# Performance work log

Hardware: AMD Instinct MI355X
Metric: run time of the kernel (lower is better)

Reference implementation:

```python
import jax, jax.numpy as jnp
import numpy as np

B, S, H, W = 16, 4096, 1024, 1024


def setup_inputs() -> dict:
    key = jax.random.key(0)
    k1, k2, k3 = jax.random.split(key, 3)
    hidden_states = jax.random.normal(k1, (B, S, H), dtype=jnp.float32)
    # (start, end) spans with start <= end, indices in [0, S)
    word_idxs = jnp.sort(jax.random.randint(k2, (B, W, 2), 0, S), axis=-1)
    # number of valid words per example, in [1, W]
    max_word_len = jax.random.randint(k3, (B,), 1, W + 1)
    return {"hidden_states": hidden_states, "word_idxs": word_idxs,
            "max_word_len": max_word_len}


def reference(hidden_states, word_idxs, max_word_len):
    # hidden_states: (B, S, H); word_idxs: (B, W, 2) int; max_word_len: (B,) int
    b, s, h = hidden_states.shape
    w = word_idxs.shape[1]
    start = word_idxs[..., 0]                      # (B, W)
    end = word_idxs[..., 1]                        # (B, W)
    pos = jnp.arange(s)                            # (S,)
    # word k is valid iff k < max_word_len[b]
    valid = (jnp.arange(w)[None, :] < max_word_len[:, None])   # (B, W) bool
    # dense mean-pooling matrix: 1/len inside [start, end], 0 elsewhere
    inside = (pos[None, None, :] >= start[..., None]) & \
             (pos[None, None, :] <= end[..., None])            # (B, W, S)
    length = (end - start + 1).astype(hidden_states.dtype)     # >= 1 by construction
    pool = inside.astype(hidden_states.dtype) / length[..., None]
    pool = pool * valid[..., None].astype(hidden_states.dtype)
    word_embedding = jnp.einsum('bws,bsh->bwh', pool, hidden_states)
    word_masks = valid.astype(jnp.int64)
    return word_embedding, word_masks
```

## Files before the change

kernel.cpp:

```cpp
#include <hip/hip_runtime.h>

static constexpr int B = 16, S = 4096, H = 1024, W = 1024;
static constexpr int NC = 64;
static constexpr int CS = S / NC;
static constexpr int LOG2_CS = 6;
static constexpr int BMW = S / 32;

__global__ void k_bitset(const int* __restrict__ widx, const int* __restrict__ mwl,
                         unsigned* __restrict__ bm) {
    int tid = blockIdx.x * 256 + threadIdx.x;
    if (tid >= B * W) return;
    int b = tid / W, w = tid % W;
    if (w >= mwl[b]) return;
    int start = widx[tid * 2 + 0];
    int end   = widx[tid * 2 + 1];
    atomicOr(&bm[b * BMW + (end >> 5)], 1u << (end & 31));
    if (start > 0) {
        int sm = start - 1;
        atomicOr(&bm[b * BMW + (sm >> 5)], 1u << (sm & 31));
    }
}

__global__ void __launch_bounds__(256)
k_chunk_prefix(const float* __restrict__ hs, const unsigned* __restrict__ bm,
               float* __restrict__ L, float* __restrict__ CTraw) {
    int c = blockIdx.x % NC;
    int b = blockIdx.x / NC;
    int col = threadIdx.x * 4;
    size_t rowbase = ((size_t)b * S + (size_t)c * CS) * H + col;
    unsigned bw0 = bm[b * BMW + c * 2 + 0];
    unsigned bw1 = bm[b * BMW + c * 2 + 1];
    float4 acc = make_float4(0.f, 0.f, 0.f, 0.f);
#pragma unroll 8
    for (int s = 0; s < CS; ++s) {
        float4 v = *(const float4*)(hs + rowbase + (size_t)s * H);
        acc.x += v.x; acc.y += v.y; acc.z += v.z; acc.w += v.w;
        unsigned bits = (s < 32) ? (bw0 >> s) : (bw1 >> (s - 32));
        if (bits & 1u)
            *(float4*)(L + rowbase + (size_t)s * H) = acc;
    }
    *(float4*)(CTraw + ((size_t)b * NC + c) * H + col) = acc;
}

__global__ void k_coarse(const float* __restrict__ CTraw, float* __restrict__ CTp) {
    int hc = blockIdx.x % (H / 256);
    int b  = blockIdx.x / (H / 256);
    int h  = hc * 256 + threadIdx.x;
    float acc = 0.f;
#pragma unroll 8
    for (int c = 0; c < NC; ++c) {
        size_t idx = ((size_t)b * NC + c) * H + h;
        CTp[idx] = acc;
        acc += CTraw[idx];
    }
}

__global__ void __launch_bounds__(256)
k_gather(const float* __restrict__ L, const float* __restrict__ CTp,
         const int* __restrict__ widx, const int* __restrict__ mwl,
         float* __restrict__ out, float* __restrict__ mask) {
    int t = threadIdx.x;
    int wid = t >> 6, lane = t & 63;
    int word = blockIdx.x * 4 + wid;
    int b = word / W, w = word % W;
    size_t orow = (size_t)word * H;

    bool valid = (w < mwl[b]);
    if (lane == 0) mask[word] = valid ? 1.0f : 0.0f;

    if (!valid) {
        float4 z = make_float4(0.f, 0.f, 0.f, 0.f);
#pragma unroll
        for (int k = 0; k < 4; ++k)
            *(float4*)(out + orow + k * 256 + lane * 4) = z;
        return;
    }

    int start = widx[word * 2 + 0];
    int end   = widx[word * 2 + 1];
    float inv = 1.0f / (float)(end - start + 1);
    int ce = end >> LOG2_CS;
    const float* Le = L   + ((size_t)b * S + end) * H;
    const float* Ce = CTp + ((size_t)b * NC + ce) * H;
    bool has_s = (start > 0);
    const float* Ls = Le; const float* Cs = Ce;
    if (has_s) {
        int sm = start - 1, cs = sm >> LOG2_CS;
        Ls = L   + ((size_t)b * S + sm) * H;
        Cs = CTp + ((size_t)b * NC + cs) * H;
    }

#pragma unroll
    for (int k = 0; k < 4; ++k) {
        int off = k * 256 + lane * 4;
        float4 e  = *(const float4*)(Le + off);
        float4 ct = *(const float4*)(Ce + off);
        float sx = e.x + ct.x, sy = e.y + ct.y, sz = e.z + ct.z, sw = e.w + ct.w;
        if (has_s) {
            float4 s4 = *(const float4*)(Ls + off);
            float4 c4 = *(const float4*)(Cs + off);
            sx -= s4.x + c4.x; sy -= s4.y + c4.y; sz -= s4.z + c4.z; sw -= s4.w + c4.w;
        }
        float4 o = make_float4(sx * inv, sy * inv, sz * inv, sw * inv);
        *(float4*)(out + orow + off) = o;
    }
}

__global__ void k_direct(const float* __restrict__ hs, const int* __restrict__ widx,
                         const int* __restrict__ mwl, float* __restrict__ out,
                         float* __restrict__ mask) {
    int w = blockIdx.x % W;
    int b = blockIdx.x / W;
    int t = threadIdx.x;
    bool valid = (w < mwl[b]);
    size_t orow = ((size_t)b * W + w) * H;
    if (t == 0) mask[(size_t)b * W + w] = valid ? 1.0f : 0.0f;

    float4 acc = make_float4(0.f, 0.f, 0.f, 0.f);
    if (valid) {
        int start = widx[((size_t)b * W + w) * 2 + 0];
        int end   = widx[((size_t)b * W + w) * 2 + 1];
        float inv = 1.0f / (float)(end - start + 1);
        for (int s = start; s <= end; ++s) {
            const float4 v = *(const float4*)(hs + ((size_t)b * S + s) * H + (size_t)t * 4);
            acc.x += v.x; acc.y += v.y; acc.z += v.z; acc.w += v.w;
        }
        acc.x *= inv; acc.y *= inv; acc.z *= inv; acc.w *= inv;
    }
    *(float4*)(out + orow + (size_t)t * 4) = acc;
}

extern "C" void kernel_launch(void* const* d_in, const int* in_sizes, int n_in,
                              void* d_out, int out_size, void* d_ws, size_t ws_size,
                              hipStream_t stream) {
    const float* hs  = (const float*)d_in[0];
    const int*  widx = (const int*)d_in[1];
    const int*  mwl  = (const int*)d_in[2];
    float* out  = (float*)d_out;
    float* mask = out + (size_t)B * W * H;

    const size_t Lbytes  = (size_t)B * S * H * sizeof(float);
    const size_t CTbytes = (size_t)B * NC * H * sizeof(float);
    const size_t BMbytes = (size_t)B * BMW * sizeof(unsigned);

    if (ws_size >= Lbytes + 2 * CTbytes + BMbytes) {
        float* L      = (float*)d_ws;
        float* CTraw  = (float*)((char*)d_ws + Lbytes);
        float* CTp    = (float*)((char*)d_ws + Lbytes + CTbytes);
        unsigned* bm  = (unsigned*)((char*)d_ws + Lbytes + 2 * CTbytes);

        hipMemsetAsync(bm, 0, BMbytes, stream);
        hipLaunchKernelGGL(k_bitset,       dim3((B * W + 255) / 256), dim3(256), 0, stream,
                           widx, mwl, bm);
        hipLaunchKernelGGL(k_chunk_prefix, dim3(B * NC),              dim3(256), 0, stream,
                           hs, bm, L, CTraw);
        hipLaunchKernelGGL(k_coarse,       dim3(B * (H / 256)),       dim3(256), 0, stream,
                           CTraw, CTp);
        hipLaunchKernelGGL(k_gather,       dim3(B * W / 4),           dim3(256), 0, stream,
                           L, CTp, widx, mwl, out, mask);
    } else {
        hipLaunchKernelGGL(k_direct, dim3(B * W), dim3(256), 0, stream, hs, widx, mwl, out, mask);
    }
}
```

Before: 113.5 us.

## Halve chunk size, build bitset in shared memory, prefix coarse sums in place

Doubles the number of chunks (NC 64→128, chunk size 32), so the prefix kernel launches twice as many blocks and each thread does a shorter serial loop with a single bitmap word. The bitset kernel now runs one block per batch, does its atomics in LDS and writes the bitmap directly, which removes the memset call. The coarse scan now works in place on one CT buffer. In exchange the coarse scan has a longer serial loop over 128 chunks, and the bitset step has only 16 blocks.

```diff
diff --git a/kernel.cpp b/kernel.cpp
--- a/kernel.cpp
+++ b/kernel.cpp
@@ -1,62 +1,72 @@
 #include <hip/hip_runtime.h>
 
+typedef float f4 __attribute__((ext_vector_type(4)));
+
 static constexpr int B = 16, S = 4096, H = 1024, W = 1024;
-static constexpr int NC = 64;
+static constexpr int NC = 128;
 static constexpr int CS = S / NC;
-static constexpr int LOG2_CS = 6;
+static constexpr int LOG2_CS = 5;
 static constexpr int BMW = S / 32;
 
-__global__ void k_bitset(const int* __restrict__ widx, const int* __restrict__ mwl,
-                         unsigned* __restrict__ bm) {
-    int tid = blockIdx.x * 256 + threadIdx.x;
-    if (tid >= B * W) return;
-    int b = tid / W, w = tid % W;
-    if (w >= mwl[b]) return;
-    int start = widx[tid * 2 + 0];
-    int end   = widx[tid * 2 + 1];
-    atomicOr(&bm[b * BMW + (end >> 5)], 1u << (end & 31));
-    if (start > 0) {
-        int sm = start - 1;
-        atomicOr(&bm[b * BMW + (sm >> 5)], 1u << (sm & 31));
+__global__ void __launch_bounds__(256)
+k_bitset(const int* __restrict__ widx, const int* __restrict__ mwl,
+         unsigned* __restrict__ bm) {
+    __shared__ unsigned lbm[BMW];
+    int b = blockIdx.x, t = threadIdx.x;
+    for (int i = t; i < BMW; i += 256) lbm[i] = 0u;
+    __syncthreads();
+    int nv = mwl[b];
+    for (int w = t; w < W; w += 256) {
+        if (w < nv) {
+            int start = widx[((size_t)b * W + w) * 2 + 0];
+            int end   = widx[((size_t)b * W + w) * 2 + 1];
+            atomicOr(&lbm[end >> 5], 1u << (end & 31));
+            if (start > 0) {
+                int sm = start - 1;
+                atomicOr(&lbm[sm >> 5], 1u << (sm & 31));
+            }
+        }
+    }
+    __syncthreads();
+    for (int i = t; i < BMW; i += 256) bm[b * BMW + i] = lbm[i];
+}
+
+__global__ void __launch_bounds__(256)
+k_prefix(const float* __restrict__ hs, const unsigned* __restrict__ bm,
+         float* __restrict__ L, float* __restrict__ CT) {
+    int c = blockIdx.x % NC;
+    int b = blockIdx.x / NC;
+    int col = threadIdx.x * 4;
+    size_t rowbase = ((size_t)b * S + (size_t)c * CS) * H + col;
+    unsigned bw = bm[b * BMW + c];
+    f4 acc = {0.f, 0.f, 0.f, 0.f};
+#pragma unroll 8
+    for (int s = 0; s < CS; ++s) {
+        f4 v = *(const f4*)(hs + rowbase + (size_t)s * H);
+        acc += v;
+        if ((bw >> s) & 1u)
+            *(f4*)(L + rowbase + (size_t)s * H) = acc;
+    }
+    *(f4*)(CT + ((size_t)b * NC + c) * H + col) = acc;
+}
+
+__global__ void __launch_bounds__(256)
+k_coarse(float* __restrict__ CT) {
+    int hq = blockIdx.x % (H / 256);
+    int b  = blockIdx.x / (H / 256);
+    int h  = hq * 256 + threadIdx.x;
+    float acc = 0.f;
+#pragma unroll 8
+    for (int c = 0; c < NC; ++c) {
+        size_t idx = ((size_t)b * NC + c) * H + h;
+        float v = CT[idx];
+        CT[idx] = acc;
+        acc += v;
     }
 }
 
 __global__ void __launch_bounds__(256)
-k_chunk_prefix(const float* __restrict__ hs, const unsigned* __restrict__ bm,
-               float* __restrict__ L, float* __restrict__ CTraw) {
-    int c = blockIdx.x % NC;
-    int b = blockIdx.x / NC;
-    int col = threadIdx.x * 4;
-    size_t rowbase = ((size_t)b * S + (size_t)c * CS) * H + col;
-    unsigned bw0 = bm[b * BMW + c * 2 + 0];
-    unsigned bw1 = bm[b * BMW + c * 2 + 1];
-    float4 acc = make_float4(0.f, 0.f, 0.f, 0.f);
-#pragma unroll 8
-    for (int s = 0; s < CS; ++s) {
-        float4 v = *(const float4*)(hs + rowbase + (size_t)s * H);
-        acc.x += v.x; acc.y += v.y; acc.z += v.z; acc.w += v.w;
-        unsigned bits = (s < 32) ? (bw0 >> s) : (bw1 >> (s - 32));
-        if (bits & 1u)
-            *(float4*)(L + rowbase + (size_t)s * H) = acc;
-    }
-    *(float4*)(CTraw + ((size_t)b * NC + c) * H + col) = acc;
-}
-
-__global__ void k_coarse(const float* __restrict__ CTraw, float* __restrict__ CTp) {
-    int hc = blockIdx.x % (H / 256);
-    int b  = blockIdx.x / (H / 256);
-    int h  = hc * 256 + threadIdx.x;
-    float acc = 0.f;
-#pragma unroll 8
-    for (int c = 0; c < NC; ++c) {
-        size_t idx = ((size_t)b * NC + c) * H + h;
-        CTp[idx] = acc;
-        acc += CTraw[idx];
-    }
-}
-
-__global__ void __launch_bounds__(256)
-k_gather(const float* __restrict__ L, const float* __restrict__ CTp,
+k_gather(const float* __restrict__ L, const float* __restrict__ CT,
          const int* __restrict__ widx, const int* __restrict__ mwl,
          float* __restrict__ out, float* __restrict__ mask) {
     int t = threadIdx.x;
@@ -69,40 +79,40 @@
     if (lane == 0) mask[word] = valid ? 1.0f : 0.0f;
 
     if (!valid) {
-        float4 z = make_float4(0.f, 0.f, 0.f, 0.f);
+        f4 z = {0.f, 0.f, 0.f, 0.f};
 #pragma unroll
         for (int k = 0; k < 4; ++k)
-            *(float4*)(out + orow + k * 256 + lane * 4) = z;
+            *(f4*)(out + orow + k * 256 + lane * 4) = z;
         return;
     }
 
-    int start = widx[word * 2 + 0];
-    int end   = widx[word * 2 + 1];
+    int start = widx[(size_t)word * 2 + 0];
+    int end   = widx[(size_t)word * 2 + 1];
     float inv = 1.0f / (float)(end - start + 1);
     int ce = end >> LOG2_CS;
-    const float* Le = L   + ((size_t)b * S + end) * H;
-    const float* Ce = CTp + ((size_t)b * NC + ce) * H;
+    const float* Le = L  + ((size_t)b * S + end) * H;
+    const float* Ce = CT + ((size_t)b * NC + ce) * H;
     bool has_s = (start > 0);
     const float* Ls = Le; const float* Cs = Ce;
     if (has_s) {
         int sm = start - 1, cs = sm >> LOG2_CS;
-        Ls = L   + ((size_t)b * S + sm) * H;
-        Cs = CTp + ((size_t)b * NC + cs) * H;
+        Ls = L  + ((size_t)b * S + sm) * H;
+        Cs = CT + ((size_t)b * NC + cs) * H;
     }
 
 #pragma unroll
     for (int k = 0; k < 4; ++k) {
         int off = k * 256 + lane * 4;
-        float4 e  = *(const float4*)(Le + off);
-        float4 ct = *(const float4*)(Ce + off);
-        float sx = e.x + ct.x, sy = e.y + ct.y, sz = e.z + ct.z, sw = e.w + ct.w;
+        f4 e  = *(const f4*)(Le + off);
+        f4 ct = *(const f4*)(Ce + off);
+        f4 ssum = e + ct;
         if (has_s) {
-            float4 s4 = *(const float4*)(Ls + off);
-            float4 c4 = *(const float4*)(Cs + off);
-            sx -= s4.x + c4.x; sy -= s4.y + c4.y; sz -= s4.z + c4.z; sw -= s4.w + c4.w;
+            f4 s4 = *(const f4*)(Ls + off);
+            f4 c4 = *(const f4*)(Cs + off);
+            ssum -= s4 + c4;
         }
-        float4 o = make_float4(sx * inv, sy * inv, sz * inv, sw * inv);
-        *(float4*)(out + orow + off) = o;
+        f4 o = ssum * inv;
+        *(f4*)(out + orow + off) = o;
     }
 }
 
@@ -116,18 +126,18 @@
     size_t orow = ((size_t)b * W + w) * H;
     if (t == 0) mask[(size_t)b * W + w] = valid ? 1.0f : 0.0f;
 
-    float4 acc = make_float4(0.f, 0.f, 0.f, 0.f);
+    f4 acc = {0.f, 0.f, 0.f, 0.f};
     if (valid) {
         int start = widx[((size_t)b * W + w) * 2 + 0];
         int end   = widx[((size_t)b * W + w) * 2 + 1];
         float inv = 1.0f / (float)(end - start + 1);
         for (int s = start; s <= end; ++s) {
-            const float4 v = *(const float4*)(hs + ((size_t)b * S + s) * H + (size_t)t * 4);
-            acc.x += v.x; acc.y += v.y; acc.z += v.z; acc.w += v.w;
+            f4 v = *(const f4*)(hs + ((size_t)b * S + s) * H + (size_t)t * 4);
+            acc += v;
         }
-        acc.x *= inv; acc.y *= inv; acc.z *= inv; acc.w *= inv;
+        acc *= inv;
     }
-    *(float4*)(out + orow + (size_t)t * 4) = acc;
+    *(f4*)(out + orow + (size_t)t * 4) = acc;
 }
 
 extern "C" void kernel_launch(void* const* d_in, const int* in_sizes, int n_in,
@@ -143,21 +153,16 @@
     const size_t CTbytes = (size_t)B * NC * H * sizeof(float);
     const size_t BMbytes = (size_t)B * BMW * sizeof(unsigned);
 
-    if (ws_size >= Lbytes + 2 * CTbytes + BMbytes) {
-        float* L      = (float*)d_ws;
-        float* CTraw  = (float*)((char*)d_ws + Lbytes);
-        float* CTp    = (float*)((char*)d_ws + Lbytes + CTbytes);
-        unsigned* bm  = (unsigned*)((char*)d_ws + Lbytes + 2 * CTbytes);
+    if (ws_size >= Lbytes + CTbytes + BMbytes) {
+        float* L     = (float*)d_ws;
+        float* CT    = (float*)((char*)d_ws + Lbytes);
+        unsigned* bm = (unsigned*)((char*)d_ws + Lbytes + CTbytes);
 
-        hipMemsetAsync(bm, 0, BMbytes, stream);
-        hipLaunchKernelGGL(k_bitset,       dim3((B * W + 255) / 256), dim3(256), 0, stream,
-                           widx, mwl, bm);
-        hipLaunchKernelGGL(k_chunk_prefix, dim3(B * NC),              dim3(256), 0, stream,
-                           hs, bm, L, CTraw);
-        hipLaunchKernelGGL(k_coarse,       dim3(B * (H / 256)),       dim3(256), 0, stream,
-                           CTraw, CTp);
-        hipLaunchKernelGGL(k_gather,       dim3(B * W / 4),           dim3(256), 0, stream,
-                           L, CTp, widx, mwl, out, mask);
+        hipLaunchKernelGGL(k_bitset, dim3(B),               dim3(256), 0, stream, widx, mwl, bm);
+        hipLaunchKernelGGL(k_prefix, dim3(B * NC),          dim3(256), 0, stream, hs, bm, L, CT);
+        hipLaunchKernelGGL(k_coarse, dim3(B * (H / 256)),   dim3(256), 0, stream, CT);
+        hipLaunchKernelGGL(k_gather, dim3(B * W / 4),       dim3(256), 0, stream,
+                           L, CT, widx, mwl, out, mask);
     } else {
         hipLaunchKernelGGL(k_direct, dim3(B * W), dim3(256), 0, stream, hs, widx, mwl, out, mask);
     }
```

New measurement: 110.6 us. 1.03x faster.
